# Kernel optimization log

Hardware: AMD Instinct MI355X
Metric: run time of the kernel (lower is better)

The kernel has to match this reference:

```python
import jax, jax.numpy as jnp
import numpy as np

OUT_F, IN_F, GS = 11008, 4096, 64        # out_features, in_features, group_size
TOKENS = 4096
G = OUT_F * IN_F // GS                    # number of quantization groups = 704512


def setup_inputs() -> dict:
    key = jax.random.key(0)
    k1, k2, k3, k4, k5 = jax.random.split(key, 5)
    x = jax.random.normal(k1, (TOKENS, IN_F), dtype=jnp.float32)
    # packed 4-bit weights: two 4-bit values per byte (high nibble = first half rows)
    W_q = jax.random.randint(k2, (GS // 2, G), 0, 256, dtype=jnp.int32)
    # per-group dequant params: scale = 1/s (small positive), zero in [0, 15]
    scale = jax.random.uniform(k3, (1, G), dtype=jnp.float32, minval=1e-3, maxval=1e-2)
    zero = jax.random.uniform(k4, (1, G), dtype=jnp.float32, minval=0.0, maxval=15.0)
    bias = jax.random.normal(k5, (OUT_F,), dtype=jnp.float32) * 0.01
    return {"x": x, "W_q": W_q, "scale": scale, "zero": zero, "bias": bias}


def _dequantize(W_q, scale, zero):
    # BitPack.unpack_4bit_u8: first half of rows from high nibble, second half from low nibble
    hi = ((W_q >> 4) & 0xF).astype(jnp.float32)   # [GS//2, G]
    lo = (W_q & 0xF).astype(jnp.float32)          # [GS//2, G]
    W_r = jnp.concatenate([hi, lo], axis=0)       # [GS, G]
    # (W_r - zero) * scale, then reshape back to the original weight shape
    return ((W_r - zero) * scale).reshape(OUT_F, IN_F)


def reference(x, W_q, scale, zero, bias):
    # HQQMatmulNoCacheDeq.forward: out = x @ dequantize().T + bias
    W = _dequantize(W_q, scale, zero)             # [OUT_F, IN_F]
    return x @ W.T + bias                         # [TOKENS, OUT_F]
```

## Files before the change

### kernel.cpp

```cpp
#include <hip/hip_runtime.h>

#define TOK  4096
#define INF  4096
#define OUTF 11008
#define NG   704512
#define QD   172

typedef __bf16 bf16x8 __attribute__((ext_vector_type(8)));
typedef float  floatx4 __attribute__((ext_vector_type(4)));

__device__ inline void glds16(const __bf16* g, __bf16* l) {
  __builtin_amdgcn_global_load_lds(
      (const __attribute__((address_space(1))) void*)g,
      (__attribute__((address_space(3))) void*)l,
      16, 0, 0);
}

__global__ __launch_bounds__(256) void convert_x_kernel(
    const float* __restrict__ x, __bf16* __restrict__ Xb) {
  size_t i = ((size_t)blockIdx.x * 256 + threadIdx.x) * 8;
  float4 a = *(const float4*)(x + i);
  float4 b = *(const float4*)(x + i + 4);
  bf16x8 o;
  o[0] = (__bf16)a.x; o[1] = (__bf16)a.y; o[2] = (__bf16)a.z; o[3] = (__bf16)a.w;
  o[4] = (__bf16)b.x; o[5] = (__bf16)b.y; o[6] = (__bf16)b.z; o[7] = (__bf16)b.w;
  *(bf16x8*)(Xb + i) = o;
}

__global__ __launch_bounds__(256) void dequant_w_kernel(
    const int* __restrict__ Wq, const float* __restrict__ sc,
    const float* __restrict__ zp, __bf16* __restrict__ Wb) {
  const int b = blockIdx.x;
  const int r = b / QD;
  const int q = b - r * QD;
  const int*   wrow = Wq + (size_t)r * NG + (size_t)q * INF;
  const float* srow = sc + (size_t)q * INF;
  const float* zrow = zp + (size_t)q * INF;
  __bf16* hrow = Wb + (size_t)(r * QD + q) * INF;
  __bf16* lrow = Wb + (size_t)((r + 32) * QD + q) * INF;
#pragma unroll
  for (int it = 0; it < 2; ++it) {
    const int k = ((int)threadIdx.x + it * 256) * 8;
    int4   w0 = *(const int4*)(wrow + k);
    int4   w1 = *(const int4*)(wrow + k + 4);
    float4 s0 = *(const float4*)(srow + k);
    float4 s1 = *(const float4*)(srow + k + 4);
    float4 z0 = *(const float4*)(zrow + k);
    float4 z1 = *(const float4*)(zrow + k + 4);
    bf16x8 hi, lo;
    hi[0] = (__bf16)(((float)((w0.x >> 4) & 0xF) - z0.x) * s0.x);
    hi[1] = (__bf16)(((float)((w0.y >> 4) & 0xF) - z0.y) * s0.y);
    hi[2] = (__bf16)(((float)((w0.z >> 4) & 0xF) - z0.z) * s0.z);
    hi[3] = (__bf16)(((float)((w0.w >> 4) & 0xF) - z0.w) * s0.w);
    hi[4] = (__bf16)(((float)((w1.x >> 4) & 0xF) - z1.x) * s1.x);
    hi[5] = (__bf16)(((float)((w1.y >> 4) & 0xF) - z1.y) * s1.y);
    hi[6] = (__bf16)(((float)((w1.z >> 4) & 0xF) - z1.z) * s1.z);
    hi[7] = (__bf16)(((float)((w1.w >> 4) & 0xF) - z1.w) * s1.w);
    lo[0] = (__bf16)(((float)(w0.x & 0xF) - z0.x) * s0.x);
    lo[1] = (__bf16)(((float)(w0.y & 0xF) - z0.y) * s0.y);
    lo[2] = (__bf16)(((float)(w0.z & 0xF) - z0.z) * s0.z);
    lo[3] = (__bf16)(((float)(w0.w & 0xF) - z0.w) * s0.w);
    lo[4] = (__bf16)(((float)(w1.x & 0xF) - z1.x) * s1.x);
    lo[5] = (__bf16)(((float)(w1.y & 0xF) - z1.y) * s1.y);
    lo[6] = (__bf16)(((float)(w1.z & 0xF) - z1.z) * s1.z);
    lo[7] = (__bf16)(((float)(w1.w & 0xF) - z1.w) * s1.w);
    *(bf16x8*)(hrow + k) = hi;
    *(bf16x8*)(lrow + k) = lo;
  }
}


#define MM_QUARTER(A_, JX, MOFF)                                              \
    _Pragma("unroll") for (int mi = 0; mi < 4; ++mi)                          \
      afr[mi] = *(const bf16x8*)((A_) + aoff + ((mi + (MOFF)) << 10) + (JX)); \
    __builtin_amdgcn_s_setprio(1);                                            \
    _Pragma("unroll") for (int mi = 0; mi < 4; ++mi)                          \
      _Pragma("unroll") for (int ni = 0; ni < 4; ++ni)                        \
        acc[mi + (MOFF)][ni] = __builtin_amdgcn_mfma_f32_16x16x32_bf16(       \
            afr[mi], bfr[ni], acc[mi + (MOFF)][ni], 0, 0, 0);                 \
    __builtin_amdgcn_s_setprio(0);

#define KTILE_COMPUTE(BUF)                                                    \
  { const __bf16* A_ = &As[BUF][0];                                           \
    const __bf16* B_ = &Bs[BUF][0];                                           \
    bf16x8 afr[4], bfr[4];                                                    \
    _Pragma("unroll") for (int ni = 0; ni < 4; ++ni)                          \
      bfr[ni] = *(const bf16x8*)(B_ + boff + (ni << 10) + jx0);               \
    MM_QUARTER(A_, jx0, 0)                                                    \
    MM_QUARTER(A_, jx0, 4)                                                    \
    _Pragma("unroll") for (int ni = 0; ni < 4; ++ni)                          \
      bfr[ni] = *(const bf16x8*)(B_ + boff + (ni << 10) + jx1);               \
    MM_QUARTER(A_, jx1, 0)                                                    \
    MM_QUARTER(A_, jx1, 4)                                                    \
  }

#define KTILE_SYNC(BUF, DO_STAGE, KOFF2, VMC)                                 \
    asm volatile("s_waitcnt lgkmcnt(0)" ::: "memory");                        \
    __builtin_amdgcn_s_barrier();                                             \
    asm volatile("" ::: "memory");                                            \
    if (DO_STAGE) {                                                           \
      _Pragma("unroll") for (int r = 0; r < 4; ++r)                           \
        glds16(gA[r] + (KOFF2), (BUF) ? lA1[r] : lA0[r]);                     \
      _Pragma("unroll") for (int r = 0; r < 4; ++r)                           \
        glds16(gB[r] + (KOFF2), (BUF) ? lB1[r] : lB0[r]);                     \
    }                                                                         \
    if ((VMC) == 8) { asm volatile("s_waitcnt vmcnt(8)" ::: "memory"); }      \
    else            { asm volatile("s_waitcnt vmcnt(0)" ::: "memory"); }      \
    __builtin_amdgcn_s_barrier();                                             \
    asm volatile("" ::: "memory");

__global__ __launch_bounds__(512, 2) void gemm_bt(
    const __bf16* __restrict__ Xb, const __bf16* __restrict__ Wb,
    const float* __restrict__ bias, float* __restrict__ out) {
  __shared__ __align__(16) __bf16 As[2][256 * 64];
  __shared__ __align__(16) __bf16 Bs[2][256 * 64];

  const int tid  = threadIdx.x;
  const int wave = tid >> 6;
  const int lane = tid & 63;

  const int orig = blockIdx.x;
  const int swz  = (orig & 7) * 86 + (orig >> 3);
  const int bn   = swz % 43;
  const int bm   = swz / 43;
  const int m0   = bm << 8;
  const int n0   = bn << 8;

  const int wm = (wave >> 2) << 7;
  const int wn = (wave & 3) << 6;

  const __bf16* gA[4]; const __bf16* gB[4];
  __bf16 *lA0[4], *lB0[4], *lA1[4], *lB1[4];
#pragma unroll
  for (int r = 0; r < 4; ++r) {
    const int c   = (r << 9) + tid;
    const int row = c >> 3;
    const int j   = (c & 7) ^ (row & 7);
    gA[r] = Xb + (size_t)(m0 + row) * INF + (j << 3);
    gB[r] = Wb + (size_t)(n0 + row) * INF + (j << 3);
    const int lbase = ((r << 9) + (wave << 6)) << 3;
    lA0[r] = &As[0][lbase]; lA1[r] = &As[1][lbase];
    lB0[r] = &Bs[0][lbase]; lB1[r] = &Bs[1][lbase];
  }

#pragma unroll
  for (int r = 0; r < 4; ++r) glds16(gA[r], lA0[r]);
#pragma unroll
  for (int r = 0; r < 4; ++r) glds16(gB[r], lB0[r]);
#pragma unroll
  for (int r = 0; r < 4; ++r) glds16(gA[r] + 64, lA1[r]);
#pragma unroll
  for (int r = 0; r < 4; ++r) glds16(gB[r] + 64, lB1[r]);

  floatx4 acc[8][4];
  const floatx4 z4 = {0.f, 0.f, 0.f, 0.f};
#pragma unroll
  for (int mi = 0; mi < 8; ++mi)
#pragma unroll
    for (int ni = 0; ni < 4; ++ni) acc[mi][ni] = z4;

  const int fr   = lane & 15;
  const int quad = lane >> 4;
  const int jx0  = ((0 * 4 + quad) ^ (fr & 7)) << 3;
  const int jx1  = ((1 * 4 + quad) ^ (fr & 7)) << 3;
  const int aoff = (wm + fr) << 6;
  const int boff = (wn + fr) << 6;

  asm volatile("s_waitcnt vmcnt(8)" ::: "memory");
  __builtin_amdgcn_s_barrier();
  asm volatile("" ::: "memory");

  for (int t = 0; t < 62; t += 2) {
    KTILE_COMPUTE(0) KTILE_SYNC(0, 1, ((t + 2) << 6), 8)
    KTILE_COMPUTE(1) KTILE_SYNC(1, 1, ((t + 3) << 6), 8)
  }
  KTILE_COMPUTE(0) KTILE_SYNC(0, 0, 0, 0)
  KTILE_COMPUTE(1)

#pragma unroll
  for (int ni = 0; ni < 4; ++ni) {
    const int n = n0 + wn + (ni << 4) + fr;
    const float bv = bias[n];
#pragma unroll
    for (int mi = 0; mi < 8; ++mi) {
      const int mb = m0 + wm + (mi << 4) + (quad << 2);
#pragma unroll
      for (int j = 0; j < 4; ++j) {
        out[(size_t)(mb + j) * OUTF + n] = acc[mi][ni][j] + bv;
      }
    }
  }
}

extern "C" void kernel_launch(void* const* d_in, const int* in_sizes, int n_in,
                              void* d_out, int out_size, void* d_ws, size_t ws_size,
                              hipStream_t stream) {
  const float* x  = (const float*)d_in[0];
  const int*   Wq = (const int*)d_in[1];
  const float* sc = (const float*)d_in[2];
  const float* zp = (const float*)d_in[3];
  const float* bs = (const float*)d_in[4];
  float* out = (float*)d_out;

  __bf16* Xb = (__bf16*)d_ws;
  __bf16* Wb = Xb + (size_t)TOK * INF;

  convert_x_kernel<<<dim3((TOK * INF) / (256 * 8)), dim3(256), 0, stream>>>(x, Xb);
  dequant_w_kernel<<<dim3(32 * QD), dim3(256), 0, stream>>>(Wq, sc, zp, Wb);
  gemm_bt<<<dim3(OUTF / 256 * (TOK / 256)), dim3(512), 0, stream>>>(Xb, Wb, bs, out);
}
```

Before: 688.0 us.

## Interleave next-tile global-to-LDS loads with MFMA quarters and remap block tiles per XCD

Restructures the GEMM main loop so that loads for the next K tile are issued in pieces between the MFMA quarters of the current tile, instead of in one burst after a barrier. The previous design used two barriers per tile and a prefetch depth of two. The new one uses a one-tile-ahead double buffer with partial vmcnt waits, and assigns staging rows per wave so each wave loads contiguous 8-row strips. It also replaces the block swizzle with an explicit per-XCD mapping that gives each XCD a compact group of N-columns and M-rows, aiming at better L2 reuse. The shallower prefetch could expose more memory latency, and the hand-tuned vmcnt counts are fragile.

```diff
diff --git a/kernel.cpp b/kernel.cpp
--- a/kernel.cpp
+++ b/kernel.cpp
@@ -70,44 +70,46 @@
 }
 
 
-#define MM_QUARTER(A_, JX, MOFF)                                              \
-    _Pragma("unroll") for (int mi = 0; mi < 4; ++mi)                          \
-      afr[mi] = *(const bf16x8*)((A_) + aoff + ((mi + (MOFF)) << 10) + (JX)); \
-    __builtin_amdgcn_s_setprio(1);                                            \
-    _Pragma("unroll") for (int mi = 0; mi < 4; ++mi)                          \
-      _Pragma("unroll") for (int ni = 0; ni < 4; ++ni)                        \
-        acc[mi + (MOFF)][ni] = __builtin_amdgcn_mfma_f32_16x16x32_bf16(       \
-            afr[mi], bfr[ni], acc[mi + (MOFF)][ni], 0, 0, 0);                 \
+#define QUAD(MOFF, JX)                                                       \
+    _Pragma("unroll") for (int mi = 0; mi < 4; ++mi)                         \
+      af[mi] = *(const bf16x8*)(A_ + aoff + ((mi + (MOFF)) << 10) + (JX));   \
+    __builtin_amdgcn_s_setprio(1);                                           \
+    _Pragma("unroll") for (int mi = 0; mi < 4; ++mi)                         \
+      _Pragma("unroll") for (int ni = 0; ni < 4; ++ni)                       \
+        acc[mi + (MOFF)][ni] = __builtin_amdgcn_mfma_f32_16x16x32_bf16(      \
+            af[mi], bfr[ni], acc[mi + (MOFF)][ni], 0, 0, 0);                 \
     __builtin_amdgcn_s_setprio(0);
 
-#define KTILE_COMPUTE(BUF)                                                    \
-  { const __bf16* A_ = &As[BUF][0];                                           \
-    const __bf16* B_ = &Bs[BUF][0];                                           \
-    bf16x8 afr[4], bfr[4];                                                    \
-    _Pragma("unroll") for (int ni = 0; ni < 4; ++ni)                          \
-      bfr[ni] = *(const bf16x8*)(B_ + boff + (ni << 10) + jx0);               \
-    MM_QUARTER(A_, jx0, 0)                                                    \
-    MM_QUARTER(A_, jx0, 4)                                                    \
-    _Pragma("unroll") for (int ni = 0; ni < 4; ++ni)                          \
-      bfr[ni] = *(const bf16x8*)(B_ + boff + (ni << 10) + jx1);               \
-    MM_QUARTER(A_, jx1, 0)                                                    \
-    MM_QUARTER(A_, jx1, 4)                                                    \
-  }
-
-#define KTILE_SYNC(BUF, DO_STAGE, KOFF2, VMC)                                 \
-    asm volatile("s_waitcnt lgkmcnt(0)" ::: "memory");                        \
-    __builtin_amdgcn_s_barrier();                                             \
-    asm volatile("" ::: "memory");                                            \
-    if (DO_STAGE) {                                                           \
-      _Pragma("unroll") for (int r = 0; r < 4; ++r)                           \
-        glds16(gA[r] + (KOFF2), (BUF) ? lA1[r] : lA0[r]);                     \
-      _Pragma("unroll") for (int r = 0; r < 4; ++r)                           \
-        glds16(gB[r] + (KOFF2), (BUF) ? lB1[r] : lB0[r]);                     \
-    }                                                                         \
-    if ((VMC) == 8) { asm volatile("s_waitcnt vmcnt(8)" ::: "memory"); }      \
-    else            { asm volatile("s_waitcnt vmcnt(0)" ::: "memory"); }      \
-    __builtin_amdgcn_s_barrier();                                             \
-    asm volatile("" ::: "memory");
+#define TILE(P_, Q_, T_)                                                     \
+  { const __bf16* A_ = &As[P_][0];                                           \
+    const __bf16* B_ = &Bs[P_][0];                                           \
+    const int st_ = (T_) < 63;                                               \
+    const int ks_ = ((T_) + 1) << 6;                                         \
+    bf16x8 af[4], bfr[4];                                                    \
+    _Pragma("unroll") for (int ni = 0; ni < 4; ++ni)                         \
+      bfr[ni] = *(const bf16x8*)(B_ + boff + (ni << 10) + jx0);              \
+    if (st_) { glds16(sgB[0] + ks_, lB##Q_[0]);                              \
+               glds16(sgB[1] + ks_, lB##Q_[1]);                              \
+               asm volatile("s_waitcnt vmcnt(2)" ::: "memory"); }            \
+    else     { asm volatile("s_waitcnt vmcnt(0)" ::: "memory"); }            \
+    __builtin_amdgcn_s_barrier();                                            \
+    asm volatile("" ::: "memory");                                           \
+    QUAD(0, jx0)                                                             \
+    if (st_) { glds16(sgB[2] + ks_, lB##Q_[2]);                              \
+               glds16(sgB[3] + ks_, lB##Q_[3]); }                            \
+    QUAD(4, jx0)                                                             \
+    if (st_) { glds16(sgA[0] + ks_, lA##Q_[0]);                              \
+               glds16(sgA[1] + ks_, lA##Q_[1]); }                            \
+    _Pragma("unroll") for (int ni = 0; ni < 4; ++ni)                         \
+      bfr[ni] = *(const bf16x8*)(B_ + boff + (ni << 10) + jx1);              \
+    QUAD(0, jx1)                                                             \
+    if (st_) { glds16(sgA[2] + ks_, lA##Q_[2]);                              \
+               glds16(sgA[3] + ks_, lA##Q_[3]); }                            \
+    QUAD(4, jx1)                                                             \
+    if (st_) { asm volatile("s_waitcnt vmcnt(4)" ::: "memory");              \
+               __builtin_amdgcn_s_barrier();                                 \
+               asm volatile("" ::: "memory"); }                              \
+  }
 
 __global__ __launch_bounds__(512, 2) void gemm_bt(
     const __bf16* __restrict__ Xb, const __bf16* __restrict__ Wb,
@@ -120,37 +122,40 @@
   const int lane = tid & 63;
 
   const int orig = blockIdx.x;
-  const int swz  = (orig & 7) * 86 + (orig >> 3);
-  const int bn   = swz % 43;
-  const int bm   = swz / 43;
-  const int m0   = bm << 8;
-  const int n0   = bn << 8;
+  const int xcd  = orig & 7;
+  const int slot = orig >> 3;
+  int bm, bn;
+  if (slot < 64) {
+    bm = ((slot >> 5) << 3) + (slot & 7);
+    bn = xcd * 5 + ((slot >> 3) & 3);
+  } else if (slot < 80) {
+    bm = slot - 64;
+    bn = xcd * 5 + 4;
+  } else {
+    const int idx = xcd * 6 + (slot - 80);
+    bm = idx & 15;
+    bn = 40 + (idx >> 4);
+  }
+  const int m0 = bm << 8;
+  const int n0 = bn << 8;
 
   const int wm = (wave >> 2) << 7;
   const int wn = (wave & 3) << 6;
 
-  const __bf16* gA[4]; const __bf16* gB[4];
-  __bf16 *lA0[4], *lB0[4], *lA1[4], *lB1[4];
-#pragma unroll
-  for (int r = 0; r < 4; ++r) {
-    const int c   = (r << 9) + tid;
-    const int row = c >> 3;
-    const int j   = (c & 7) ^ (row & 7);
-    gA[r] = Xb + (size_t)(m0 + row) * INF + (j << 3);
-    gB[r] = Wb + (size_t)(n0 + row) * INF + (j << 3);
-    const int lbase = ((r << 9) + (wave << 6)) << 3;
-    lA0[r] = &As[0][lbase]; lA1[r] = &As[1][lbase];
-    lB0[r] = &Bs[0][lbase]; lB1[r] = &Bs[1][lbase];
-  }
-
-#pragma unroll
-  for (int r = 0; r < 4; ++r) glds16(gA[r], lA0[r]);
-#pragma unroll
-  for (int r = 0; r < 4; ++r) glds16(gB[r], lB0[r]);
-#pragma unroll
-  for (int r = 0; r < 4; ++r) glds16(gA[r] + 64, lA1[r]);
-#pragma unroll
-  for (int r = 0; r < 4; ++r) glds16(gB[r] + 64, lB1[r]);
+  const int hA = wave >> 2, u = wave & 3;
+  const int hB = (wave & 3) >> 1, v = ((wave >> 2) << 1) | (wave & 1);
+  const int jst = (lane & 7) ^ (lane >> 3);
+  const __bf16* sgA[4]; const __bf16* sgB[4];
+  __bf16 *lA0[4], *lA1[4], *lB0[4], *lB1[4];
+#pragma unroll
+  for (int i = 0; i < 4; ++i) {
+    const int ra = hA * 128 + u * 32 + i * 8;
+    const int rb = hB * 128 + v * 32 + i * 8;
+    sgA[i] = Xb + (size_t)(m0 + ra + (lane >> 3)) * INF + (jst << 3);
+    sgB[i] = Wb + (size_t)(n0 + rb + (lane >> 3)) * INF + (jst << 3);
+    lA0[i] = &As[0][ra << 6]; lA1[i] = &As[1][ra << 6];
+    lB0[i] = &Bs[0][rb << 6]; lB1[i] = &Bs[1][rb << 6];
+  }
 
   floatx4 acc[8][4];
   const floatx4 z4 = {0.f, 0.f, 0.f, 0.f};
@@ -166,16 +171,18 @@
   const int aoff = (wm + fr) << 6;
   const int boff = (wn + fr) << 6;
 
-  asm volatile("s_waitcnt vmcnt(8)" ::: "memory");
+#pragma unroll
+  for (int i = 0; i < 4; ++i) glds16(sgB[i], lB0[i]);
+#pragma unroll
+  for (int i = 0; i < 4; ++i) glds16(sgA[i], lA0[i]);
+  asm volatile("s_waitcnt vmcnt(4)" ::: "memory");
   __builtin_amdgcn_s_barrier();
   asm volatile("" ::: "memory");
 
-  for (int t = 0; t < 62; t += 2) {
-    KTILE_COMPUTE(0) KTILE_SYNC(0, 1, ((t + 2) << 6), 8)
-    KTILE_COMPUTE(1) KTILE_SYNC(1, 1, ((t + 3) << 6), 8)
-  }
-  KTILE_COMPUTE(0) KTILE_SYNC(0, 0, 0, 0)
-  KTILE_COMPUTE(1)
+  for (int t = 0; t < 64; t += 2) {
+    TILE(0, 1, t)
+    TILE(1, 0, t + 1)
+  }
 
 #pragma unroll
   for (int ni = 0; ni < 4; ++ni) {
```

Result: slower. 724.3 us (+5.3%).

## Interleave global-to-LDS staging across four MFMA phases and remap tiles per XCD

Applied to the files above, without the earlier changes.

Restructures the GEMM main loop into four phases per K-tile. Each phase issues a slice of the next tile's global_load_lds transfers, synchronises with barriers, and waits on partial vmcnt counts, so memory traffic overlaps MFMA work instead of being issued in one burst per tile. The prologue now stages only one tile ahead rather than two. Block-to-tile mapping is also changed so each XCD gets a contiguous band of N tiles, aiming for better L2 reuse of weight rows. The cost is more barriers per tile and a tighter, riskier wait-count scheme.

```diff
diff --git a/kernel.cpp b/kernel.cpp
--- a/kernel.cpp
+++ b/kernel.cpp
@@ -70,44 +70,52 @@
 }
 
 
-#define MM_QUARTER(A_, JX, MOFF)                                              \
+#define PHASE(A_, B_, MH, JX, NEWB, STAGE, WAITC)                             \
+  {                                                                           \
+    bf16x8 af[4];                                                             \
+    if (NEWB) {                                                               \
+      _Pragma("unroll") for (int ni = 0; ni < 4; ++ni)                        \
+        bfr[ni] = *(const bf16x8*)((B_) + boff + (ni << 10) + (JX));          \
+    }                                                                         \
     _Pragma("unroll") for (int mi = 0; mi < 4; ++mi)                          \
-      afr[mi] = *(const bf16x8*)((A_) + aoff + ((mi + (MOFF)) << 10) + (JX)); \
+      af[mi] = *(const bf16x8*)((A_) + aoff + (((MH) * 4 + mi) << 10) + (JX));\
+    STAGE                                                                     \
+    asm volatile("" ::: "memory");                                            \
+    __builtin_amdgcn_s_barrier();                                             \
+    asm volatile("s_waitcnt lgkmcnt(0)" ::: "memory");                        \
+    __builtin_amdgcn_sched_barrier(0);                                        \
     __builtin_amdgcn_s_setprio(1);                                            \
     _Pragma("unroll") for (int mi = 0; mi < 4; ++mi)                          \
       _Pragma("unroll") for (int ni = 0; ni < 4; ++ni)                        \
-        acc[mi + (MOFF)][ni] = __builtin_amdgcn_mfma_f32_16x16x32_bf16(       \
-            afr[mi], bfr[ni], acc[mi + (MOFF)][ni], 0, 0, 0);                 \
-    __builtin_amdgcn_s_setprio(0);
-
-#define KTILE_COMPUTE(BUF)                                                    \
-  { const __bf16* A_ = &As[BUF][0];                                           \
-    const __bf16* B_ = &Bs[BUF][0];                                           \
-    bf16x8 afr[4], bfr[4];                                                    \
-    _Pragma("unroll") for (int ni = 0; ni < 4; ++ni)                          \
-      bfr[ni] = *(const bf16x8*)(B_ + boff + (ni << 10) + jx0);               \
-    MM_QUARTER(A_, jx0, 0)                                                    \
-    MM_QUARTER(A_, jx0, 4)                                                    \
-    _Pragma("unroll") for (int ni = 0; ni < 4; ++ni)                          \
-      bfr[ni] = *(const bf16x8*)(B_ + boff + (ni << 10) + jx1);               \
-    MM_QUARTER(A_, jx1, 0)                                                    \
-    MM_QUARTER(A_, jx1, 4)                                                    \
-  }
-
-#define KTILE_SYNC(BUF, DO_STAGE, KOFF2, VMC)                                 \
-    asm volatile("s_waitcnt lgkmcnt(0)" ::: "memory");                        \
+        acc[((MH) << 2) + mi][ni] = __builtin_amdgcn_mfma_f32_16x16x32_bf16(  \
+            af[mi], bfr[ni], acc[((MH) << 2) + mi][ni], 0, 0, 0);             \
+    __builtin_amdgcn_s_setprio(0);                                            \
+    WAITC                                                                     \
+    asm volatile("" ::: "memory");                                            \
     __builtin_amdgcn_s_barrier();                                             \
     asm volatile("" ::: "memory");                                            \
-    if (DO_STAGE) {                                                           \
-      _Pragma("unroll") for (int r = 0; r < 4; ++r)                           \
-        glds16(gA[r] + (KOFF2), (BUF) ? lA1[r] : lA0[r]);                     \
-      _Pragma("unroll") for (int r = 0; r < 4; ++r)                           \
-        glds16(gB[r] + (KOFF2), (BUF) ? lB1[r] : lB0[r]);                     \
-    }                                                                         \
-    if ((VMC) == 8) { asm volatile("s_waitcnt vmcnt(8)" ::: "memory"); }      \
-    else            { asm volatile("s_waitcnt vmcnt(0)" ::: "memory"); }      \
-    __builtin_amdgcn_s_barrier();                                             \
-    asm volatile("" ::: "memory");
+  }
+
+#define TILE(P_, Q_, KOFF, ST_, LAST_)                                        \
+  { const __bf16* A_ = &As[P_][0];                                            \
+    const __bf16* B_ = &Bs[P_][0];                                            \
+    bf16x8 bfr[4];                                                            \
+    PHASE(A_, B_, 0, jx0, 1,                                                  \
+      if (ST_) { glds16(gB[0] + (KOFF), lB##Q_[0]);                           \
+                 glds16(gB[1] + (KOFF), lB##Q_[1]); },                        \
+      if (LAST_) { asm volatile("s_waitcnt vmcnt(0)" ::: "memory"); }         \
+      else       { asm volatile("s_waitcnt vmcnt(2)" ::: "memory"); })        \
+    PHASE(A_, B_, 1, jx0, 0,                                                  \
+      if (ST_) { glds16(gB[2] + (KOFF), lB##Q_[2]);                           \
+                 glds16(gB[3] + (KOFF), lB##Q_[3]); }, )                      \
+    PHASE(A_, B_, 0, jx1, 1,                                                  \
+      if (ST_) { glds16(gA[0] + (KOFF), lA##Q_[0]);                           \
+                 glds16(gA[2] + (KOFF), lA##Q_[2]); }, )                      \
+    PHASE(A_, B_, 1, jx1, 0,                                                  \
+      if (ST_) { glds16(gA[1] + (KOFF), lA##Q_[1]);                           \
+                 glds16(gA[3] + (KOFF), lA##Q_[3]);                           \
+                 asm volatile("s_waitcnt vmcnt(2)" ::: "memory"); }, )        \
+  }
 
 __global__ __launch_bounds__(512, 2) void gemm_bt(
     const __bf16* __restrict__ Xb, const __bf16* __restrict__ Wb,
@@ -120,17 +128,28 @@
   const int lane = tid & 63;
 
   const int orig = blockIdx.x;
-  const int swz  = (orig & 7) * 86 + (orig >> 3);
-  const int bn   = swz % 43;
-  const int bm   = swz / 43;
-  const int m0   = bm << 8;
-  const int n0   = bn << 8;
+  const int xcd  = orig & 7;
+  const int slot = orig >> 3;
+  int bm, bn;
+  if (slot < 64) {
+    bm = ((slot >> 5) << 3) + (slot & 7);
+    bn = xcd * 5 + ((slot >> 3) & 3);
+  } else if (slot < 80) {
+    bm = slot - 64;
+    bn = xcd * 5 + 4;
+  } else {
+    const int idx = xcd * 6 + (slot - 80);
+    bm = idx & 15;
+    bn = 40 + (idx >> 4);
+  }
+  const int m0 = bm << 8;
+  const int n0 = bn << 8;
 
   const int wm = (wave >> 2) << 7;
   const int wn = (wave & 3) << 6;
 
   const __bf16* gA[4]; const __bf16* gB[4];
-  __bf16 *lA0[4], *lB0[4], *lA1[4], *lB1[4];
+  __bf16 *lA0[4], *lA1[4], *lB0[4], *lB1[4];
 #pragma unroll
   for (int r = 0; r < 4; ++r) {
     const int c   = (r << 9) + tid;
@@ -143,15 +162,6 @@
     lB0[r] = &Bs[0][lbase]; lB1[r] = &Bs[1][lbase];
   }
 
-#pragma unroll
-  for (int r = 0; r < 4; ++r) glds16(gA[r], lA0[r]);
-#pragma unroll
-  for (int r = 0; r < 4; ++r) glds16(gB[r], lB0[r]);
-#pragma unroll
-  for (int r = 0; r < 4; ++r) glds16(gA[r] + 64, lA1[r]);
-#pragma unroll
-  for (int r = 0; r < 4; ++r) glds16(gB[r] + 64, lB1[r]);
-
   floatx4 acc[8][4];
   const floatx4 z4 = {0.f, 0.f, 0.f, 0.f};
 #pragma unroll
@@ -166,16 +176,20 @@
   const int aoff = (wm + fr) << 6;
   const int boff = (wn + fr) << 6;
 
-  asm volatile("s_waitcnt vmcnt(8)" ::: "memory");
+  glds16(gB[0], lB0[0]); glds16(gB[1], lB0[1]);
+  glds16(gB[2], lB0[2]); glds16(gB[3], lB0[3]);
+  glds16(gA[0], lA0[0]); glds16(gA[2], lA0[2]);
+  glds16(gA[1], lA0[1]); glds16(gA[3], lA0[3]);
+  asm volatile("s_waitcnt vmcnt(2)" ::: "memory");
   __builtin_amdgcn_s_barrier();
   asm volatile("" ::: "memory");
 
   for (int t = 0; t < 62; t += 2) {
-    KTILE_COMPUTE(0) KTILE_SYNC(0, 1, ((t + 2) << 6), 8)
-    KTILE_COMPUTE(1) KTILE_SYNC(1, 1, ((t + 3) << 6), 8)
-  }
-  KTILE_COMPUTE(0) KTILE_SYNC(0, 0, 0, 0)
-  KTILE_COMPUTE(1)
+    TILE(0, 1, ((t + 1) << 6), 1, 0)
+    TILE(1, 0, ((t + 2) << 6), 1, 0)
+  }
+  TILE(0, 1, (63 << 6), 1, 0)
+  TILE(1, 0, 0, 0, 1)
 
 #pragma unroll
   for (int ni = 0; ni < 4; ++ni) {
```

Result: faster. 670.6 us (-2.5%).
